# Optimization experiments

Hardware: AMD Instinct MI355X
Metric: run time of the kernel (lower is better)

## Reference

```python
import jax, jax.numpy as jnp
import numpy as np

NUM_NODE = 8192
N_PTS = 20000
FEAT_DIM = 32
POS_THRESH = 0.1
NEG_THRESH = 1.4
POS_RADIUS = 0.0375   # hardcoded literal in the original forward
NEG_RADIUS = 0.1      # hardcoded literal in the original forward
BIG = 100000.0
EPS = 1e-7


def setup_inputs() -> dict:
    key = jax.random.key(0)
    k1, k2, k3, k4, k5, k6, k7 = jax.random.split(key, 7)
    # points in a small box so pos (<0.0375) and neg (>0.1) masks are both populated
    src_pcd = jax.random.uniform(k1, (N_PTS, 3), dtype=jnp.float32) * 0.2
    tgt_pcd = jax.random.uniform(k2, (N_PTS, 3), dtype=jnp.float32) * 0.2
    src_feats = jax.random.normal(k3, (N_PTS, FEAT_DIM), dtype=jnp.float32)
    tgt_feats = jax.random.normal(k4, (N_PTS, FEAT_DIM), dtype=jnp.float32)
    correspondence = jax.random.randint(k5, (NUM_NODE, 2), 0, N_PTS, dtype=jnp.int64)
    # near-identity rigid transform so transformed src stays in the same scale regime
    rot = jnp.eye(3, dtype=jnp.float32) + 0.01 * jax.random.normal(k6, (3, 3), dtype=jnp.float32)
    trans = 0.01 * jax.random.normal(k7, (3, 1), dtype=jnp.float32)
    return {
        "src_pcd": src_pcd, "tgt_pcd": tgt_pcd,
        "src_feats": src_feats, "tgt_feats": tgt_feats,
        "correspondence": correspondence, "rot": rot, "trans": trans,
    }


def _pdist_l2(A, B):
    # GEMM form of sqrt(sum((a-b)^2) + 1e-7); same math as the broadcasted original
    d2 = (jnp.sum(A * A, axis=1)[:, None]
          + jnp.sum(B * B, axis=1)[None, :]
          - 2.0 * A @ B.T)
    return jnp.sqrt(jnp.maximum(d2, 0.0) + EPS)


def reference(src_pcd, tgt_pcd, src_feats, tgt_feats, correspondence, rot, trans):
    # rigid transform of src cloud: (R @ P^T + t)^T
    src_pcd = (rot @ src_pcd.T + trans).T
    ci = correspondence[:, 0]
    cj = correspondence[:, 1]
    sel_src_pts = src_pcd[ci]       # [N,3]
    sel_tgt_pts = tgt_pcd[cj]       # [N,3]
    sel_src_feats = src_feats[ci]   # [N,D]
    sel_tgt_feats = tgt_feats[cj]   # [N,D]

    pts_dist = _pdist_l2(sel_src_pts, sel_tgt_pts)      # [N,N]
    feats_dist = _pdist_l2(sel_src_feats, sel_tgt_feats)  # [N,N]

    pos_mask = pts_dist < POS_RADIUS
    neg_mask = pts_dist > NEG_RADIUS

    furthest_positive = jnp.max(feats_dist * pos_mask.astype(feats_dist.dtype), axis=-1)
    closest_negative = jnp.min(jnp.where(neg_mask, feats_dist, BIG), axis=-1)

    pos_loss = jax.nn.relu(furthest_positive - POS_THRESH)
    neg_loss = jax.nn.relu(NEG_THRESH - closest_negative)
    loss = pos_loss.mean() + neg_loss.mean()
    return loss
```

## Files before the change

kernel.cpp:

```cpp
#include <hip/hip_runtime.h>
#include <math.h>
#include <float.h>

#define NN 8192

typedef __bf16 bf16x8 __attribute__((ext_vector_type(8)));
typedef __bf16 bf16x4 __attribute__((ext_vector_type(4)));
typedef float f32x4 __attribute__((ext_vector_type(4)));

constexpr float POS_R2 = 0.0375f * 0.0375f;
constexpr float NEG_R2 = 0.1f * 0.1f;
constexpr float EPSF = 1e-7f;
constexpr float PRC = POS_R2 - EPSF;
constexpr float NRC = NEG_R2 - EPSF;
constexpr float POS_TH = 0.1f;
constexpr float NEG_TH = 1.4f;

#define FT_OFF 0
#define FS2_OFF (NN * 64)
#define PSX_OFF (2 * NN * 64)
#define PTX_OFF (3 * NN * 64)
#define FNS_OFF (4 * NN * 64)
#define FNT_OFF (4 * NN * 64 + NN * 4)
#define MAXB_OFF (4 * NN * 64 + 2 * NN * 4)
#define MINB_OFF (4 * NN * 64 + 3 * NN * 4)

__global__ __launch_bounds__(256) void hcl_prep(
    const float* __restrict__ src_pcd, const float* __restrict__ tgt_pcd,
    const float* __restrict__ src_feats, const float* __restrict__ tgt_feats,
    const int* __restrict__ corr, const float* __restrict__ rot,
    const float* __restrict__ trans, char* __restrict__ ws) {
  int i = blockIdx.x * 256 + threadIdx.x;
  if (i >= NN) return;
  int ci = corr[2 * i];
  int cj = corr[2 * i + 1];

  float r00 = rot[0], r01 = rot[1], r02 = rot[2];
  float r10 = rot[3], r11 = rot[4], r12 = rot[5];
  float r20 = rot[6], r21 = rot[7], r22 = rot[8];
  float t0 = trans[0], t1 = trans[1], t2 = trans[2];

  float px = src_pcd[ci * 3 + 0], py = src_pcd[ci * 3 + 1], pz = src_pcd[ci * 3 + 2];
  float qx = r00 * px + r01 * py + r02 * pz + t0;
  float qy = r10 * px + r11 * py + r12 * pz + t1;
  float qz = r20 * px + r21 * py + r22 * pz + t2;
  float sa = qx * qx + qy * qy + qz * qz;

  float ux = tgt_pcd[cj * 3 + 0], uy = tgt_pcd[cj * 3 + 1], uz = tgt_pcd[cj * 3 + 2];
  float sb = ux * ux + uy * uy + uz * uz;

  __bf16 qhx = (__bf16)qx, qhy = (__bf16)qy, qhz = (__bf16)qz;
  __bf16 qlx = (__bf16)(qx - (float)qhx);
  __bf16 qly = (__bf16)(qy - (float)qhy);
  __bf16 qlz = (__bf16)(qz - (float)qhz);
  __bf16 sah = (__bf16)sa;
  __bf16 sal = (__bf16)(sa - (float)sah);

  __bf16 uhx = (__bf16)ux, uhy = (__bf16)uy, uhz = (__bf16)uz;
  __bf16 ulx = (__bf16)(ux - (float)uhx);
  __bf16 uly = (__bf16)(uy - (float)uhy);
  __bf16 ulz = (__bf16)(uz - (float)uhz);
  __bf16 sbh = (__bf16)sb;
  __bf16 sbl = (__bf16)(sb - (float)sbh);
  __bf16 m2hx = (__bf16)(-2.f * (float)uhx), m2hy = (__bf16)(-2.f * (float)uhy),
         m2hz = (__bf16)(-2.f * (float)uhz);
  __bf16 m2lx = (__bf16)(-2.f * (float)ulx), m2ly = (__bf16)(-2.f * (float)uly),
         m2lz = (__bf16)(-2.f * (float)ulz);
  __bf16 one = (__bf16)1.0f, zero = (__bf16)0.0f;

  {
    bf16x8 v0, v1, vz;
    v0[0] = qhx; v0[1] = qhy; v0[2] = qhz; v0[3] = qhx; v0[4] = qhy; v0[5] = qhz;
    v0[6] = qlx; v0[7] = qly;
    v1[0] = qlz; v1[1] = sah; v1[2] = sal; v1[3] = one; v1[4] = one;
    v1[5] = zero; v1[6] = zero; v1[7] = zero;
    for (int k = 0; k < 8; ++k) vz[k] = zero;
    bf16x8* p = (bf16x8*)(ws + PSX_OFF + (size_t)i * 64);
    p[0] = v0; p[1] = v1; p[2] = vz; p[3] = vz;
  }
  {
    bf16x8 w0, w1, wz;
    w0[0] = m2hx; w0[1] = m2hy; w0[2] = m2hz; w0[3] = m2lx; w0[4] = m2ly; w0[5] = m2lz;
    w0[6] = m2hx; w0[7] = m2hy;
    w1[0] = m2hz; w1[1] = one; w1[2] = one; w1[3] = sbh; w1[4] = sbl;
    w1[5] = zero; w1[6] = zero; w1[7] = zero;
    for (int k = 0; k < 8; ++k) wz[k] = zero;
    bf16x8* p = (bf16x8*)(ws + PTX_OFF + (size_t)i * 64);
    p[0] = w0; p[1] = w1; p[2] = wz; p[3] = wz;
  }

  float fa = 0.f, fb = 0.f;
  const float4* sf = (const float4*)(src_feats + (size_t)ci * 32);
  const float4* tf = (const float4*)(tgt_feats + (size_t)cj * 32);
  bf16x4* ofs = (bf16x4*)(ws + FS2_OFF + (size_t)i * 64);
  bf16x4* oft = (bf16x4*)(ws + FT_OFF + (size_t)i * 64);
#pragma unroll
  for (int k = 0; k < 8; ++k) {
    float4 a = sf[k];
    __bf16 h0 = (__bf16)a.x, h1 = (__bf16)a.y, h2 = (__bf16)a.z, h3 = (__bf16)a.w;
    float f0 = (float)h0, f1 = (float)h1, f2 = (float)h2, f3 = (float)h3;
    fa += f0 * f0 + f1 * f1 + f2 * f2 + f3 * f3;
    bf16x4 o;
    o[0] = (__bf16)(-2.f * f0); o[1] = (__bf16)(-2.f * f1);
    o[2] = (__bf16)(-2.f * f2); o[3] = (__bf16)(-2.f * f3);
    ofs[k] = o;

    float4 b = tf[k];
    __bf16 g0 = (__bf16)b.x, g1 = (__bf16)b.y, g2 = (__bf16)b.z, g3 = (__bf16)b.w;
    float e0 = (float)g0, e1 = (float)g1, e2 = (float)g2, e3 = (float)g3;
    fb += e0 * e0 + e1 * e1 + e2 * e2 + e3 * e3;
    bf16x4 o2;
    o2[0] = g0; o2[1] = g1; o2[2] = g2; o2[3] = g3;
    oft[k] = o2;
  }
  ((float*)(ws + FNS_OFF))[i] = fa;
  ((float*)(ws + FNT_OFF))[i] = fb;
  ((unsigned int*)(ws + MAXB_OFF))[i] = 0u;
  ((unsigned int*)(ws + MINB_OFF))[i] = 0x7F7FFFFFu;
}

__global__ __launch_bounds__(256, 4) void hcl_dist(char* __restrict__ ws) {
  const int lane = threadIdx.x & 63;
  const int wave = threadIdx.x >> 6;
  const int quad = lane >> 4;
  const int n = lane & 15;
  const int i0 = blockIdx.y * 128 + wave * 32;
  const int j0 = blockIdx.x * 512;

  const bf16x8 afeat0 = *(const bf16x8*)(ws + FS2_OFF + (size_t)(i0 + n) * 64 + quad * 16);
  const bf16x8 afeat1 = *(const bf16x8*)(ws + FS2_OFF + (size_t)(i0 + 16 + n) * 64 + quad * 16);
  const bf16x8 apos0 = *(const bf16x8*)(ws + PSX_OFF + (size_t)(i0 + n) * 64 + quad * 16);
  const bf16x8 apos1 = *(const bf16x8*)(ws + PSX_OFF + (size_t)(i0 + 16 + n) * 64 + quad * 16);
  const f32x4 fa0 = *(const f32x4*)(ws + FNS_OFF + (size_t)(i0 + quad * 4) * 4);
  const f32x4 fa1 = *(const f32x4*)(ws + FNS_OFF + (size_t)(i0 + 16 + quad * 4) * 4);

  float maxv[8], minv[8];
#pragma unroll
  for (int r = 0; r < 8; ++r) {
    maxv[r] = -1.0f;
    minv[r] = FLT_MAX;
  }

#pragma unroll 2
  for (int s = 0; s < 32; ++s) {
    const int col = j0 + s * 16 + n;
    const bf16x8 bfeat = *(const bf16x8*)(ws + FT_OFF + (size_t)col * 64 + quad * 16);
    const bf16x8 bpos = *(const bf16x8*)(ws + PTX_OFF + (size_t)col * 64 + quad * 16);
    const float fb = *(const float*)(ws + FNT_OFF + (size_t)col * 4);

    f32x4 c0, c1, z;
    c0[0] = fa0[0] + fb; c0[1] = fa0[1] + fb; c0[2] = fa0[2] + fb; c0[3] = fa0[3] + fb;
    c1[0] = fa1[0] + fb; c1[1] = fa1[1] + fb; c1[2] = fa1[2] + fb; c1[3] = fa1[3] + fb;
    z[0] = 0.f; z[1] = 0.f; z[2] = 0.f; z[3] = 0.f;

    f32x4 d0 = __builtin_amdgcn_mfma_f32_16x16x32_bf16(afeat0, bfeat, c0, 0, 0, 0);
    f32x4 d1 = __builtin_amdgcn_mfma_f32_16x16x32_bf16(afeat1, bfeat, c1, 0, 0, 0);
    f32x4 u0 = __builtin_amdgcn_mfma_f32_16x16x32_bf16(apos0, bpos, z, 0, 0, 0);
    f32x4 u1 = __builtin_amdgcn_mfma_f32_16x16x32_bf16(apos1, bpos, z, 0, 0, 0);

#pragma unroll
    for (int r = 0; r < 4; ++r) {
      bool p0 = u0[r] < PRC, g0 = u0[r] > NRC;
      maxv[r] = fmaxf(maxv[r], p0 ? d0[r] : -1.0f);
      minv[r] = fminf(minv[r], g0 ? d0[r] : FLT_MAX);
      bool p1 = u1[r] < PRC, g1 = u1[r] > NRC;
      maxv[4 + r] = fmaxf(maxv[4 + r], p1 ? d1[r] : -1.0f);
      minv[4 + r] = fminf(minv[4 + r], g1 ? d1[r] : FLT_MAX);
    }
  }

  unsigned int* maxb = (unsigned int*)(ws + MAXB_OFF);
  unsigned int* minb = (unsigned int*)(ws + MINB_OFF);
#pragma unroll
  for (int r = 0; r < 8; ++r) {
    float mx = maxv[r], mn = minv[r];
#pragma unroll
    for (int sh = 1; sh <= 8; sh <<= 1) {
      mx = fmaxf(mx, __shfl_xor(mx, sh, 64));
      mn = fminf(mn, __shfl_xor(mn, sh, 64));
    }
    if (n == 0) {
      int row = i0 + (r < 4 ? 0 : 16) + quad * 4 + (r & 3);
      atomicMax(maxb + row, __float_as_uint(fmaxf(mx, 0.f)));
      atomicMin(minb + row, __float_as_uint(fmaxf(mn, 0.f)));
    }
  }
}

__global__ __launch_bounds__(256) void hcl_loss(const char* __restrict__ ws,
                                               float* __restrict__ out) {
  int t = threadIdx.x;
  const float* maxb = (const float*)(ws + MAXB_OFF);
  const float* minb = (const float*)(ws + MINB_OFF);
  float sp = 0.f, sn = 0.f;
#pragma unroll 8
  for (int i = t; i < NN; i += 256) {
    float fp = sqrtf(maxb[i] + EPSF);
    float cn = sqrtf(minb[i] + EPSF);
    sp += fmaxf(fp - POS_TH, 0.f);
    sn += fmaxf(NEG_TH - cn, 0.f);
  }
  __shared__ float red[8];
#pragma unroll
  for (int s = 32; s >= 1; s >>= 1) {
    sp += __shfl_down(sp, s, 64);
    sn += __shfl_down(sn, s, 64);
  }
  int wid = t >> 6;
  if ((t & 63) == 0) {
    red[wid] = sp;
    red[4 + wid] = sn;
  }
  __syncthreads();
  if (t == 0) {
    float tsp = red[0] + red[1] + red[2] + red[3];
    float tsn = red[4] + red[5] + red[6] + red[7];
    out[0] = (tsp + tsn) * (1.0f / NN);
  }
}

extern "C" void kernel_launch(void* const* d_in, const int* in_sizes, int n_in,
                              void* d_out, int out_size, void* d_ws, size_t ws_size,
                              hipStream_t stream) {
  const float* src_pcd = (const float*)d_in[0];
  const float* tgt_pcd = (const float*)d_in[1];
  const float* src_feats = (const float*)d_in[2];
  const float* tgt_feats = (const float*)d_in[3];
  const int* corr = (const int*)d_in[4];
  const float* rot = (const float*)d_in[5];
  const float* trans = (const float*)d_in[6];
  float* out = (float*)d_out;
  char* ws = (char*)d_ws;

  hcl_prep<<<NN / 256, 256, 0, stream>>>(src_pcd, tgt_pcd, src_feats, tgt_feats, corr, rot,
                                         trans, ws);
  hcl_dist<<<dim3(16, 64), 256, 0, stream>>>(ws);
  hcl_loss<<<1, 256, 0, stream>>>(ws, out);
}
```

Baseline: 104.8 us.

## Split prep work across four threads per row, unroll dist loop, vectorize loss

The prep kernel now assigns four threads to each correspondence row. Each thread converts a quarter of the features, the norms are combined with shuffles, and the point-encoding work is spread over different lanes. The dist kernel's column loop is unrolled by four with pointer increments, so loads can be issued in groups. The loss kernel reads float4 vectors. Together these aim to cut the latency of the small prep and loss kernels and the address overhead in the main loop, at the cost of some lane divergence in prep and higher register pressure in dist.

```diff
diff --git a/kernel.cpp b/kernel.cpp
--- a/kernel.cpp
+++ b/kernel.cpp
@@ -5,7 +5,6 @@
 #define NN 8192
 
 typedef __bf16 bf16x8 __attribute__((ext_vector_type(8)));
-typedef __bf16 bf16x4 __attribute__((ext_vector_type(4)));
 typedef float f32x4 __attribute__((ext_vector_type(4)));
 
 constexpr float POS_R2 = 0.0375f * 0.0375f;
@@ -30,93 +29,99 @@
     const float* __restrict__ src_feats, const float* __restrict__ tgt_feats,
     const int* __restrict__ corr, const float* __restrict__ rot,
     const float* __restrict__ trans, char* __restrict__ ws) {
-  int i = blockIdx.x * 256 + threadIdx.x;
-  if (i >= NN) return;
+  int t = blockIdx.x * 256 + threadIdx.x;
+  int i = t >> 2;
+  int p = t & 3;
   int ci = corr[2 * i];
   int cj = corr[2 * i + 1];
 
-  float r00 = rot[0], r01 = rot[1], r02 = rot[2];
-  float r10 = rot[3], r11 = rot[4], r12 = rot[5];
-  float r20 = rot[6], r21 = rot[7], r22 = rot[8];
-  float t0 = trans[0], t1 = trans[1], t2 = trans[2];
-
-  float px = src_pcd[ci * 3 + 0], py = src_pcd[ci * 3 + 1], pz = src_pcd[ci * 3 + 2];
-  float qx = r00 * px + r01 * py + r02 * pz + t0;
-  float qy = r10 * px + r11 * py + r12 * pz + t1;
-  float qz = r20 * px + r21 * py + r22 * pz + t2;
-  float sa = qx * qx + qy * qy + qz * qz;
-
-  float ux = tgt_pcd[cj * 3 + 0], uy = tgt_pcd[cj * 3 + 1], uz = tgt_pcd[cj * 3 + 2];
-  float sb = ux * ux + uy * uy + uz * uz;
-
-  __bf16 qhx = (__bf16)qx, qhy = (__bf16)qy, qhz = (__bf16)qz;
-  __bf16 qlx = (__bf16)(qx - (float)qhx);
-  __bf16 qly = (__bf16)(qy - (float)qhy);
-  __bf16 qlz = (__bf16)(qz - (float)qhz);
-  __bf16 sah = (__bf16)sa;
-  __bf16 sal = (__bf16)(sa - (float)sah);
-
-  __bf16 uhx = (__bf16)ux, uhy = (__bf16)uy, uhz = (__bf16)uz;
-  __bf16 ulx = (__bf16)(ux - (float)uhx);
-  __bf16 uly = (__bf16)(uy - (float)uhy);
-  __bf16 ulz = (__bf16)(uz - (float)uhz);
-  __bf16 sbh = (__bf16)sb;
-  __bf16 sbl = (__bf16)(sb - (float)sbh);
-  __bf16 m2hx = (__bf16)(-2.f * (float)uhx), m2hy = (__bf16)(-2.f * (float)uhy),
-         m2hz = (__bf16)(-2.f * (float)uhz);
-  __bf16 m2lx = (__bf16)(-2.f * (float)ulx), m2ly = (__bf16)(-2.f * (float)uly),
-         m2lz = (__bf16)(-2.f * (float)ulz);
+  const float4* sf = (const float4*)(src_feats + (size_t)ci * 32);
+  const float4* tf = (const float4*)(tgt_feats + (size_t)cj * 32);
+  float na = 0.f, nb = 0.f;
+  bf16x8 osrc, otgt;
+#pragma unroll
+  for (int h = 0; h < 2; ++h) {
+    float4 a = sf[2 * p + h];
+    __bf16 h0 = (__bf16)a.x, h1 = (__bf16)a.y, h2 = (__bf16)a.z, h3 = (__bf16)a.w;
+    float f0 = (float)h0, f1 = (float)h1, f2 = (float)h2, f3 = (float)h3;
+    na += f0 * f0 + f1 * f1 + f2 * f2 + f3 * f3;
+    osrc[4 * h + 0] = (__bf16)(-2.f * f0);
+    osrc[4 * h + 1] = (__bf16)(-2.f * f1);
+    osrc[4 * h + 2] = (__bf16)(-2.f * f2);
+    osrc[4 * h + 3] = (__bf16)(-2.f * f3);
+
+    float4 b = tf[2 * p + h];
+    __bf16 g0 = (__bf16)b.x, g1 = (__bf16)b.y, g2 = (__bf16)b.z, g3 = (__bf16)b.w;
+    nb += (float)g0 * (float)g0 + (float)g1 * (float)g1 + (float)g2 * (float)g2 +
+          (float)g3 * (float)g3;
+    otgt[4 * h + 0] = g0;
+    otgt[4 * h + 1] = g1;
+    otgt[4 * h + 2] = g2;
+    otgt[4 * h + 3] = g3;
+  }
+  *(bf16x8*)(ws + FS2_OFF + (size_t)i * 64 + p * 16) = osrc;
+  *(bf16x8*)(ws + FT_OFF + (size_t)i * 64 + p * 16) = otgt;
+
+  na += __shfl_xor(na, 1, 4);
+  na += __shfl_xor(na, 2, 4);
+  nb += __shfl_xor(nb, 1, 4);
+  nb += __shfl_xor(nb, 2, 4);
+
   __bf16 one = (__bf16)1.0f, zero = (__bf16)0.0f;
 
-  {
+  if (p == 0) {
+    ((float*)(ws + FNS_OFF))[i] = na;
+    ((float*)(ws + FNT_OFF))[i] = nb;
+    ((unsigned int*)(ws + MAXB_OFF))[i] = 0u;
+    ((unsigned int*)(ws + MINB_OFF))[i] = 0x7F7FFFFFu;
+  } else if (p == 1) {
+    float r00 = rot[0], r01 = rot[1], r02 = rot[2];
+    float r10 = rot[3], r11 = rot[4], r12 = rot[5];
+    float r20 = rot[6], r21 = rot[7], r22 = rot[8];
+    float t0 = trans[0], t1 = trans[1], t2 = trans[2];
+    float px = src_pcd[ci * 3 + 0], py = src_pcd[ci * 3 + 1], pz = src_pcd[ci * 3 + 2];
+    float qx = r00 * px + r01 * py + r02 * pz + t0;
+    float qy = r10 * px + r11 * py + r12 * pz + t1;
+    float qz = r20 * px + r21 * py + r22 * pz + t2;
+    float sa = qx * qx + qy * qy + qz * qz;
+    __bf16 qhx = (__bf16)qx, qhy = (__bf16)qy, qhz = (__bf16)qz;
+    __bf16 qlx = (__bf16)(qx - (float)qhx);
+    __bf16 qly = (__bf16)(qy - (float)qhy);
+    __bf16 qlz = (__bf16)(qz - (float)qhz);
+    __bf16 sah = (__bf16)sa;
+    __bf16 sal = (__bf16)(sa - (float)sah);
     bf16x8 v0, v1, vz;
     v0[0] = qhx; v0[1] = qhy; v0[2] = qhz; v0[3] = qhx; v0[4] = qhy; v0[5] = qhz;
     v0[6] = qlx; v0[7] = qly;
     v1[0] = qlz; v1[1] = sah; v1[2] = sal; v1[3] = one; v1[4] = one;
     v1[5] = zero; v1[6] = zero; v1[7] = zero;
+#pragma unroll
     for (int k = 0; k < 8; ++k) vz[k] = zero;
-    bf16x8* p = (bf16x8*)(ws + PSX_OFF + (size_t)i * 64);
-    p[0] = v0; p[1] = v1; p[2] = vz; p[3] = vz;
-  }
-  {
+    bf16x8* o = (bf16x8*)(ws + PSX_OFF + (size_t)i * 64);
+    o[0] = v0; o[1] = v1; o[2] = vz; o[3] = vz;
+  } else if (p == 2) {
+    float ux = tgt_pcd[cj * 3 + 0], uy = tgt_pcd[cj * 3 + 1], uz = tgt_pcd[cj * 3 + 2];
+    float sb = ux * ux + uy * uy + uz * uz;
+    __bf16 uhx = (__bf16)ux, uhy = (__bf16)uy, uhz = (__bf16)uz;
+    __bf16 ulx = (__bf16)(ux - (float)uhx);
+    __bf16 uly = (__bf16)(uy - (float)uhy);
+    __bf16 ulz = (__bf16)(uz - (float)uhz);
+    __bf16 sbh = (__bf16)sb;
+    __bf16 sbl = (__bf16)(sb - (float)sbh);
+    __bf16 m2hx = (__bf16)(-2.f * (float)uhx), m2hy = (__bf16)(-2.f * (float)uhy),
+           m2hz = (__bf16)(-2.f * (float)uhz);
+    __bf16 m2lx = (__bf16)(-2.f * (float)ulx), m2ly = (__bf16)(-2.f * (float)uly),
+           m2lz = (__bf16)(-2.f * (float)ulz);
     bf16x8 w0, w1, wz;
     w0[0] = m2hx; w0[1] = m2hy; w0[2] = m2hz; w0[3] = m2lx; w0[4] = m2ly; w0[5] = m2lz;
     w0[6] = m2hx; w0[7] = m2hy;
     w1[0] = m2hz; w1[1] = one; w1[2] = one; w1[3] = sbh; w1[4] = sbl;
     w1[5] = zero; w1[6] = zero; w1[7] = zero;
+#pragma unroll
     for (int k = 0; k < 8; ++k) wz[k] = zero;
-    bf16x8* p = (bf16x8*)(ws + PTX_OFF + (size_t)i * 64);
-    p[0] = w0; p[1] = w1; p[2] = wz; p[3] = wz;
-  }
-
-  float fa = 0.f, fb = 0.f;
-  const float4* sf = (const float4*)(src_feats + (size_t)ci * 32);
-  const float4* tf = (const float4*)(tgt_feats + (size_t)cj * 32);
-  bf16x4* ofs = (bf16x4*)(ws + FS2_OFF + (size_t)i * 64);
-  bf16x4* oft = (bf16x4*)(ws + FT_OFF + (size_t)i * 64);
-#pragma unroll
-  for (int k = 0; k < 8; ++k) {
-    float4 a = sf[k];
-    __bf16 h0 = (__bf16)a.x, h1 = (__bf16)a.y, h2 = (__bf16)a.z, h3 = (__bf16)a.w;
-    float f0 = (float)h0, f1 = (float)h1, f2 = (float)h2, f3 = (float)h3;
-    fa += f0 * f0 + f1 * f1 + f2 * f2 + f3 * f3;
-    bf16x4 o;
-    o[0] = (__bf16)(-2.f * f0); o[1] = (__bf16)(-2.f * f1);
-    o[2] = (__bf16)(-2.f * f2); o[3] = (__bf16)(-2.f * f3);
-    ofs[k] = o;
-
-    float4 b = tf[k];
-    __bf16 g0 = (__bf16)b.x, g1 = (__bf16)b.y, g2 = (__bf16)b.z, g3 = (__bf16)b.w;
-    float e0 = (float)g0, e1 = (float)g1, e2 = (float)g2, e3 = (float)g3;
-    fb += e0 * e0 + e1 * e1 + e2 * e2 + e3 * e3;
-    bf16x4 o2;
-    o2[0] = g0; o2[1] = g1; o2[2] = g2; o2[3] = g3;
-    oft[k] = o2;
-  }
-  ((float*)(ws + FNS_OFF))[i] = fa;
-  ((float*)(ws + FNT_OFF))[i] = fb;
-  ((unsigned int*)(ws + MAXB_OFF))[i] = 0u;
-  ((unsigned int*)(ws + MINB_OFF))[i] = 0x7F7FFFFFu;
+    bf16x8* o = (bf16x8*)(ws + PTX_OFF + (size_t)i * 64);
+    o[0] = w0; o[1] = w1; o[2] = wz; o[3] = wz;
+  }
 }
 
 __global__ __launch_bounds__(256, 4) void hcl_dist(char* __restrict__ ws) {
@@ -126,11 +131,12 @@
   const int n = lane & 15;
   const int i0 = blockIdx.y * 128 + wave * 32;
   const int j0 = blockIdx.x * 512;
-
-  const bf16x8 afeat0 = *(const bf16x8*)(ws + FS2_OFF + (size_t)(i0 + n) * 64 + quad * 16);
-  const bf16x8 afeat1 = *(const bf16x8*)(ws + FS2_OFF + (size_t)(i0 + 16 + n) * 64 + quad * 16);
-  const bf16x8 apos0 = *(const bf16x8*)(ws + PSX_OFF + (size_t)(i0 + n) * 64 + quad * 16);
-  const bf16x8 apos1 = *(const bf16x8*)(ws + PSX_OFF + (size_t)(i0 + 16 + n) * 64 + quad * 16);
+  const size_t aoff = (size_t)quad * 16;
+
+  const bf16x8 afeat0 = *(const bf16x8*)(ws + FS2_OFF + (size_t)(i0 + n) * 64 + aoff);
+  const bf16x8 afeat1 = *(const bf16x8*)(ws + FS2_OFF + (size_t)(i0 + 16 + n) * 64 + aoff);
+  const bf16x8 apos0 = *(const bf16x8*)(ws + PSX_OFF + (size_t)(i0 + n) * 64 + aoff);
+  const bf16x8 apos1 = *(const bf16x8*)(ws + PSX_OFF + (size_t)(i0 + 16 + n) * 64 + aoff);
   const f32x4 fa0 = *(const f32x4*)(ws + FNS_OFF + (size_t)(i0 + quad * 4) * 4);
   const f32x4 fa1 = *(const f32x4*)(ws + FNS_OFF + (size_t)(i0 + 16 + quad * 4) * 4);
 
@@ -141,32 +147,40 @@
     minv[r] = FLT_MAX;
   }
 
-#pragma unroll 2
-  for (int s = 0; s < 32; ++s) {
-    const int col = j0 + s * 16 + n;
-    const bf16x8 bfeat = *(const bf16x8*)(ws + FT_OFF + (size_t)col * 64 + quad * 16);
-    const bf16x8 bpos = *(const bf16x8*)(ws + PTX_OFF + (size_t)col * 64 + quad * 16);
-    const float fb = *(const float*)(ws + FNT_OFF + (size_t)col * 4);
-
-    f32x4 c0, c1, z;
-    c0[0] = fa0[0] + fb; c0[1] = fa0[1] + fb; c0[2] = fa0[2] + fb; c0[3] = fa0[3] + fb;
-    c1[0] = fa1[0] + fb; c1[1] = fa1[1] + fb; c1[2] = fa1[2] + fb; c1[3] = fa1[3] + fb;
-    z[0] = 0.f; z[1] = 0.f; z[2] = 0.f; z[3] = 0.f;
-
-    f32x4 d0 = __builtin_amdgcn_mfma_f32_16x16x32_bf16(afeat0, bfeat, c0, 0, 0, 0);
-    f32x4 d1 = __builtin_amdgcn_mfma_f32_16x16x32_bf16(afeat1, bfeat, c1, 0, 0, 0);
-    f32x4 u0 = __builtin_amdgcn_mfma_f32_16x16x32_bf16(apos0, bpos, z, 0, 0, 0);
-    f32x4 u1 = __builtin_amdgcn_mfma_f32_16x16x32_bf16(apos1, bpos, z, 0, 0, 0);
-
-#pragma unroll
-    for (int r = 0; r < 4; ++r) {
-      bool p0 = u0[r] < PRC, g0 = u0[r] > NRC;
-      maxv[r] = fmaxf(maxv[r], p0 ? d0[r] : -1.0f);
-      minv[r] = fminf(minv[r], g0 ? d0[r] : FLT_MAX);
-      bool p1 = u1[r] < PRC, g1 = u1[r] > NRC;
-      maxv[4 + r] = fmaxf(maxv[4 + r], p1 ? d1[r] : -1.0f);
-      minv[4 + r] = fminf(minv[4 + r], g1 ? d1[r] : FLT_MAX);
+  const char* pF = ws + FT_OFF + (size_t)(j0 + n) * 64 + aoff;
+  const char* pP = ws + PTX_OFF + (size_t)(j0 + n) * 64 + aoff;
+  const char* pN = ws + FNT_OFF + (size_t)(j0 + n) * 4;
+
+  for (int s = 0; s < 8; ++s) {
+#pragma unroll
+    for (int u = 0; u < 4; ++u) {
+      const bf16x8 bfeat = *(const bf16x8*)(pF + u * 1024);
+      const bf16x8 bpos = *(const bf16x8*)(pP + u * 1024);
+      const float fb = *(const float*)(pN + u * 64);
+
+      f32x4 c0, c1, z;
+      c0[0] = fa0[0] + fb; c0[1] = fa0[1] + fb; c0[2] = fa0[2] + fb; c0[3] = fa0[3] + fb;
+      c1[0] = fa1[0] + fb; c1[1] = fa1[1] + fb; c1[2] = fa1[2] + fb; c1[3] = fa1[3] + fb;
+      z[0] = 0.f; z[1] = 0.f; z[2] = 0.f; z[3] = 0.f;
+
+      f32x4 d0 = __builtin_amdgcn_mfma_f32_16x16x32_bf16(afeat0, bfeat, c0, 0, 0, 0);
+      f32x4 d1 = __builtin_amdgcn_mfma_f32_16x16x32_bf16(afeat1, bfeat, c1, 0, 0, 0);
+      f32x4 u0 = __builtin_amdgcn_mfma_f32_16x16x32_bf16(apos0, bpos, z, 0, 0, 0);
+      f32x4 u1 = __builtin_amdgcn_mfma_f32_16x16x32_bf16(apos1, bpos, z, 0, 0, 0);
+
+#pragma unroll
+      for (int r = 0; r < 4; ++r) {
+        bool p0 = u0[r] < PRC, g0 = u0[r] > NRC;
+        maxv[r] = fmaxf(maxv[r], p0 ? d0[r] : -1.0f);
+        minv[r] = fminf(minv[r], g0 ? d0[r] : FLT_MAX);
+        bool p1 = u1[r] < PRC, g1 = u1[r] > NRC;
+        maxv[4 + r] = fmaxf(maxv[4 + r], p1 ? d1[r] : -1.0f);
+        minv[4 + r] = fminf(minv[4 + r], g1 ? d1[r] : FLT_MAX);
+      }
     }
+    pF += 4096;
+    pP += 4096;
+    pN += 256;
   }
 
   unsigned int* maxb = (unsigned int*)(ws + MAXB_OFF);
@@ -190,15 +204,17 @@
 __global__ __launch_bounds__(256) void hcl_loss(const char* __restrict__ ws,
                                                float* __restrict__ out) {
   int t = threadIdx.x;
-  const float* maxb = (const float*)(ws + MAXB_OFF);
-  const float* minb = (const float*)(ws + MINB_OFF);
+  const float4* maxb = (const float4*)(ws + MAXB_OFF);
+  const float4* minb = (const float4*)(ws + MINB_OFF);
   float sp = 0.f, sn = 0.f;
-#pragma unroll 8
-  for (int i = t; i < NN; i += 256) {
-    float fp = sqrtf(maxb[i] + EPSF);
-    float cn = sqrtf(minb[i] + EPSF);
-    sp += fmaxf(fp - POS_TH, 0.f);
-    sn += fmaxf(NEG_TH - cn, 0.f);
+#pragma unroll
+  for (int k = 0; k < 8; ++k) {
+    float4 mx = maxb[t + 256 * k];
+    float4 mn = minb[t + 256 * k];
+    sp += fmaxf(sqrtf(mx.x + EPSF) - POS_TH, 0.f) + fmaxf(sqrtf(mx.y + EPSF) - POS_TH, 0.f) +
+          fmaxf(sqrtf(mx.z + EPSF) - POS_TH, 0.f) + fmaxf(sqrtf(mx.w + EPSF) - POS_TH, 0.f);
+    sn += fmaxf(NEG_TH - sqrtf(mn.x + EPSF), 0.f) + fmaxf(NEG_TH - sqrtf(mn.y + EPSF), 0.f) +
+          fmaxf(NEG_TH - sqrtf(mn.z + EPSF), 0.f) + fmaxf(NEG_TH - sqrtf(mn.w + EPSF), 0.f);
   }
   __shared__ float red[8];
 #pragma unroll
@@ -232,8 +248,8 @@
   float* out = (float*)d_out;
   char* ws = (char*)d_ws;
 
-  hcl_prep<<<NN / 256, 256, 0, stream>>>(src_pcd, tgt_pcd, src_feats, tgt_feats, corr, rot,
-                                         trans, ws);
+  hcl_prep<<<NN * 4 / 256, 256, 0, stream>>>(src_pcd, tgt_pcd, src_feats, tgt_feats, corr,
+                                             rot, trans, ws);
   hcl_dist<<<dim3(16, 64), 256, 0, stream>>>(ws);
   hcl_loss<<<1, 256, 0, stream>>>(ws, out);
 }
```

Result: faster. 100.9 us (-3.7%).

## Stage column tiles in LDS, fuse loss into dist kernel, parallelize prep

Applied to the files above, without the earlier changes.

The distance kernel now loads its 512-column tile of target features, positions and norms into LDS once per block with global_load_lds, and the inner loop reads from LDS instead of global memory. Blocks grow to 512 threads covering 256 rows. The separate loss kernel is removed: the last block to finish, chosen by an atomic ticket counter, does the final reduction. The prep kernel uses 8 threads per row, and the position buffers shrink from 64 to 32 bytes per row. This removes one launch and redundant global column loads, at the cost of a grid-wide atomic and roughly 50KB of LDS per block, which limits occupancy.

```diff
diff --git a/kernel.cpp b/kernel.cpp
--- a/kernel.cpp
+++ b/kernel.cpp
@@ -19,118 +19,151 @@
 #define FT_OFF 0
 #define FS2_OFF (NN * 64)
 #define PSX_OFF (2 * NN * 64)
-#define PTX_OFF (3 * NN * 64)
-#define FNS_OFF (4 * NN * 64)
-#define FNT_OFF (4 * NN * 64 + NN * 4)
-#define MAXB_OFF (4 * NN * 64 + 2 * NN * 4)
-#define MINB_OFF (4 * NN * 64 + 3 * NN * 4)
+#define PTX_OFF (2 * NN * 64 + NN * 32)
+#define FNS_OFF (2 * NN * 64 + 2 * NN * 32)
+#define FNT_OFF (FNS_OFF + NN * 4)
+#define MAXB_OFF (FNT_OFF + NN * 4)
+#define MINB_OFF (MAXB_OFF + NN * 4)
+#define CNT_OFF (MINB_OFF + NN * 4)
+
+__device__ inline void load_lds16(const void* g, void* l) {
+  __builtin_amdgcn_global_load_lds(
+      (const __attribute__((address_space(1))) unsigned int*)g,
+      (__attribute__((address_space(3))) unsigned int*)l, 16, 0, 0);
+}
 
 __global__ __launch_bounds__(256) void hcl_prep(
     const float* __restrict__ src_pcd, const float* __restrict__ tgt_pcd,
     const float* __restrict__ src_feats, const float* __restrict__ tgt_feats,
     const int* __restrict__ corr, const float* __restrict__ rot,
     const float* __restrict__ trans, char* __restrict__ ws) {
-  int i = blockIdx.x * 256 + threadIdx.x;
-  if (i >= NN) return;
+  int t = blockIdx.x * 256 + threadIdx.x;
+  int i = t >> 3;
+  int p = t & 7;
   int ci = corr[2 * i];
   int cj = corr[2 * i + 1];
 
-  float r00 = rot[0], r01 = rot[1], r02 = rot[2];
-  float r10 = rot[3], r11 = rot[4], r12 = rot[5];
-  float r20 = rot[6], r21 = rot[7], r22 = rot[8];
-  float t0 = trans[0], t1 = trans[1], t2 = trans[2];
-
-  float px = src_pcd[ci * 3 + 0], py = src_pcd[ci * 3 + 1], pz = src_pcd[ci * 3 + 2];
-  float qx = r00 * px + r01 * py + r02 * pz + t0;
-  float qy = r10 * px + r11 * py + r12 * pz + t1;
-  float qz = r20 * px + r21 * py + r22 * pz + t2;
-  float sa = qx * qx + qy * qy + qz * qz;
-
-  float ux = tgt_pcd[cj * 3 + 0], uy = tgt_pcd[cj * 3 + 1], uz = tgt_pcd[cj * 3 + 2];
-  float sb = ux * ux + uy * uy + uz * uz;
-
-  __bf16 qhx = (__bf16)qx, qhy = (__bf16)qy, qhz = (__bf16)qz;
-  __bf16 qlx = (__bf16)(qx - (float)qhx);
-  __bf16 qly = (__bf16)(qy - (float)qhy);
-  __bf16 qlz = (__bf16)(qz - (float)qhz);
-  __bf16 sah = (__bf16)sa;
-  __bf16 sal = (__bf16)(sa - (float)sah);
-
-  __bf16 uhx = (__bf16)ux, uhy = (__bf16)uy, uhz = (__bf16)uz;
-  __bf16 ulx = (__bf16)(ux - (float)uhx);
-  __bf16 uly = (__bf16)(uy - (float)uhy);
-  __bf16 ulz = (__bf16)(uz - (float)uhz);
-  __bf16 sbh = (__bf16)sb;
-  __bf16 sbl = (__bf16)(sb - (float)sbh);
-  __bf16 m2hx = (__bf16)(-2.f * (float)uhx), m2hy = (__bf16)(-2.f * (float)uhy),
-         m2hz = (__bf16)(-2.f * (float)uhz);
-  __bf16 m2lx = (__bf16)(-2.f * (float)ulx), m2ly = (__bf16)(-2.f * (float)uly),
-         m2lz = (__bf16)(-2.f * (float)ulz);
+  float4 a = ((const float4*)(src_feats + (size_t)ci * 32))[p];
+  float4 b = ((const float4*)(tgt_feats + (size_t)cj * 32))[p];
+  __bf16 h0 = (__bf16)a.x, h1 = (__bf16)a.y, h2 = (__bf16)a.z, h3 = (__bf16)a.w;
+  float f0 = (float)h0, f1 = (float)h1, f2 = (float)h2, f3 = (float)h3;
+  float na = f0 * f0 + f1 * f1 + f2 * f2 + f3 * f3;
+  bf16x4 osrc;
+  osrc[0] = (__bf16)(-2.f * f0); osrc[1] = (__bf16)(-2.f * f1);
+  osrc[2] = (__bf16)(-2.f * f2); osrc[3] = (__bf16)(-2.f * f3);
+  __bf16 g0 = (__bf16)b.x, g1 = (__bf16)b.y, g2 = (__bf16)b.z, g3 = (__bf16)b.w;
+  float e0 = (float)g0, e1 = (float)g1, e2 = (float)g2, e3 = (float)g3;
+  float nb = e0 * e0 + e1 * e1 + e2 * e2 + e3 * e3;
+  bf16x4 otgt;
+  otgt[0] = g0; otgt[1] = g1; otgt[2] = g2; otgt[3] = g3;
+  *(bf16x4*)(ws + FS2_OFF + (size_t)i * 64 + p * 8) = osrc;
+  *(bf16x4*)(ws + FT_OFF + (size_t)i * 64 + p * 8) = otgt;
+
+  na += __shfl_xor(na, 1, 8);
+  na += __shfl_xor(na, 2, 8);
+  na += __shfl_xor(na, 4, 8);
+  nb += __shfl_xor(nb, 1, 8);
+  nb += __shfl_xor(nb, 2, 8);
+  nb += __shfl_xor(nb, 4, 8);
+
   __bf16 one = (__bf16)1.0f, zero = (__bf16)0.0f;
 
-  {
-    bf16x8 v0, v1, vz;
+  if (p == 0) {
+    ((float*)(ws + FNS_OFF))[i] = na;
+    ((float*)(ws + FNT_OFF))[i] = nb;
+    ((unsigned int*)(ws + MAXB_OFF))[i] = 0u;
+    ((unsigned int*)(ws + MINB_OFF))[i] = 0x7F7FFFFFu;
+  } else if (p == 3) {
+    if (i == 0) *(unsigned int*)(ws + CNT_OFF) = 0u;
+  } else if (p == 1) {
+    float r00 = rot[0], r01 = rot[1], r02 = rot[2];
+    float r10 = rot[3], r11 = rot[4], r12 = rot[5];
+    float r20 = rot[6], r21 = rot[7], r22 = rot[8];
+    float t0 = trans[0], t1 = trans[1], t2 = trans[2];
+    float px = src_pcd[ci * 3 + 0], py = src_pcd[ci * 3 + 1], pz = src_pcd[ci * 3 + 2];
+    float qx = r00 * px + r01 * py + r02 * pz + t0;
+    float qy = r10 * px + r11 * py + r12 * pz + t1;
+    float qz = r20 * px + r21 * py + r22 * pz + t2;
+    float sa = qx * qx + qy * qy + qz * qz;
+    __bf16 qhx = (__bf16)qx, qhy = (__bf16)qy, qhz = (__bf16)qz;
+    __bf16 qlx = (__bf16)(qx - (float)qhx);
+    __bf16 qly = (__bf16)(qy - (float)qhy);
+    __bf16 qlz = (__bf16)(qz - (float)qhz);
+    __bf16 sah = (__bf16)sa;
+    __bf16 sal = (__bf16)(sa - (float)sah);
+    bf16x8 v0, v1;
     v0[0] = qhx; v0[1] = qhy; v0[2] = qhz; v0[3] = qhx; v0[4] = qhy; v0[5] = qhz;
     v0[6] = qlx; v0[7] = qly;
     v1[0] = qlz; v1[1] = sah; v1[2] = sal; v1[3] = one; v1[4] = one;
     v1[5] = zero; v1[6] = zero; v1[7] = zero;
-    for (int k = 0; k < 8; ++k) vz[k] = zero;
-    bf16x8* p = (bf16x8*)(ws + PSX_OFF + (size_t)i * 64);
-    p[0] = v0; p[1] = v1; p[2] = vz; p[3] = vz;
-  }
-  {
-    bf16x8 w0, w1, wz;
+    bf16x8* o = (bf16x8*)(ws + PSX_OFF + (size_t)i * 32);
+    o[0] = v0;
+    o[1] = v1;
+  } else if (p == 2) {
+    float ux = tgt_pcd[cj * 3 + 0], uy = tgt_pcd[cj * 3 + 1], uz = tgt_pcd[cj * 3 + 2];
+    float sb = ux * ux + uy * uy + uz * uz;
+    __bf16 uhx = (__bf16)ux, uhy = (__bf16)uy, uhz = (__bf16)uz;
+    __bf16 ulx = (__bf16)(ux - (float)uhx);
+    __bf16 uly = (__bf16)(uy - (float)uhy);
+    __bf16 ulz = (__bf16)(uz - (float)uhz);
+    __bf16 sbh = (__bf16)sb;
+    __bf16 sbl = (__bf16)(sb - (float)sbh);
+    __bf16 m2hx = (__bf16)(-2.f * (float)uhx), m2hy = (__bf16)(-2.f * (float)uhy),
+           m2hz = (__bf16)(-2.f * (float)uhz);
+    __bf16 m2lx = (__bf16)(-2.f * (float)ulx), m2ly = (__bf16)(-2.f * (float)uly),
+           m2lz = (__bf16)(-2.f * (float)ulz);
+    bf16x8 w0, w1;
     w0[0] = m2hx; w0[1] = m2hy; w0[2] = m2hz; w0[3] = m2lx; w0[4] = m2ly; w0[5] = m2lz;
     w0[6] = m2hx; w0[7] = m2hy;
     w1[0] = m2hz; w1[1] = one; w1[2] = one; w1[3] = sbh; w1[4] = sbl;
     w1[5] = zero; w1[6] = zero; w1[7] = zero;
-    for (int k = 0; k < 8; ++k) wz[k] = zero;
-    bf16x8* p = (bf16x8*)(ws + PTX_OFF + (size_t)i * 64);
-    p[0] = w0; p[1] = w1; p[2] = wz; p[3] = wz;
-  }
-
-  float fa = 0.f, fb = 0.f;
-  const float4* sf = (const float4*)(src_feats + (size_t)ci * 32);
-  const float4* tf = (const float4*)(tgt_feats + (size_t)cj * 32);
-  bf16x4* ofs = (bf16x4*)(ws + FS2_OFF + (size_t)i * 64);
-  bf16x4* oft = (bf16x4*)(ws + FT_OFF + (size_t)i * 64);
-#pragma unroll
-  for (int k = 0; k < 8; ++k) {
-    float4 a = sf[k];
-    __bf16 h0 = (__bf16)a.x, h1 = (__bf16)a.y, h2 = (__bf16)a.z, h3 = (__bf16)a.w;
-    float f0 = (float)h0, f1 = (float)h1, f2 = (float)h2, f3 = (float)h3;
-    fa += f0 * f0 + f1 * f1 + f2 * f2 + f3 * f3;
-    bf16x4 o;
-    o[0] = (__bf16)(-2.f * f0); o[1] = (__bf16)(-2.f * f1);
-    o[2] = (__bf16)(-2.f * f2); o[3] = (__bf16)(-2.f * f3);
-    ofs[k] = o;
-
-    float4 b = tf[k];
-    __bf16 g0 = (__bf16)b.x, g1 = (__bf16)b.y, g2 = (__bf16)b.z, g3 = (__bf16)b.w;
-    float e0 = (float)g0, e1 = (float)g1, e2 = (float)g2, e3 = (float)g3;
-    fb += e0 * e0 + e1 * e1 + e2 * e2 + e3 * e3;
-    bf16x4 o2;
-    o2[0] = g0; o2[1] = g1; o2[2] = g2; o2[3] = g3;
-    oft[k] = o2;
-  }
-  ((float*)(ws + FNS_OFF))[i] = fa;
-  ((float*)(ws + FNT_OFF))[i] = fb;
-  ((unsigned int*)(ws + MAXB_OFF))[i] = 0u;
-  ((unsigned int*)(ws + MINB_OFF))[i] = 0x7F7FFFFFu;
-}
-
-__global__ __launch_bounds__(256, 4) void hcl_dist(char* __restrict__ ws) {
-  const int lane = threadIdx.x & 63;
-  const int wave = threadIdx.x >> 6;
-  const int quad = lane >> 4;
-  const int n = lane & 15;
-  const int i0 = blockIdx.y * 128 + wave * 32;
+    bf16x8* o = (bf16x8*)(ws + PTX_OFF + (size_t)i * 32);
+    o[0] = w0;
+    o[1] = w1;
+  }
+}
+
+__global__ __launch_bounds__(512, 4) void hcl_dist(char* __restrict__ ws,
+                                                   float* __restrict__ out) {
+  __shared__ char ldsF[32768];
+  __shared__ char ldsP[16384 + 64];
+  __shared__ char ldsN[2048];
+  __shared__ unsigned int s_ticket;
+  __shared__ float red[16];
+
+  const int tid = threadIdx.x;
+  const int lane = tid & 63, wv = tid >> 6;
+  const int quad = lane >> 4, n = lane & 15;
+  const int i0 = blockIdx.y * 256 + wv * 32;
   const int j0 = blockIdx.x * 512;
 
+  {
+    const char* gF = ws + FT_OFF + (size_t)j0 * 64;
+    const char* gP = ws + PTX_OFF + (size_t)j0 * 32;
+    const char* gN = ws + FNT_OFF + (size_t)j0 * 4;
+#pragma unroll
+    for (int r = 0; r < 4; ++r) {
+      int off = wv * 1024 + r * 8192;
+      load_lds16(gF + off + lane * 16, ldsF + off);
+    }
+#pragma unroll
+    for (int r = 0; r < 2; ++r) {
+      int off = wv * 1024 + r * 8192;
+      load_lds16(gP + off + lane * 16, ldsP + off);
+    }
+    if (wv == 0) load_lds16(gN + lane * 16, ldsN);
+    if (wv == 1) load_lds16(gN + 1024 + lane * 16, ldsN + 1024);
+  }
+  if (tid < 4) ((f32x4*)(ldsP + 16384))[tid] = f32x4{0.f, 0.f, 0.f, 0.f};
+
   const bf16x8 afeat0 = *(const bf16x8*)(ws + FS2_OFF + (size_t)(i0 + n) * 64 + quad * 16);
-  const bf16x8 afeat1 = *(const bf16x8*)(ws + FS2_OFF + (size_t)(i0 + 16 + n) * 64 + quad * 16);
-  const bf16x8 apos0 = *(const bf16x8*)(ws + PSX_OFF + (size_t)(i0 + n) * 64 + quad * 16);
-  const bf16x8 apos1 = *(const bf16x8*)(ws + PSX_OFF + (size_t)(i0 + 16 + n) * 64 + quad * 16);
+  const bf16x8 afeat1 =
+      *(const bf16x8*)(ws + FS2_OFF + (size_t)(i0 + 16 + n) * 64 + quad * 16);
+  bf16x8 apos0 = {}, apos1 = {};
+  if (quad < 2) {
+    apos0 = *(const bf16x8*)(ws + PSX_OFF + (size_t)(i0 + n) * 32 + quad * 16);
+    apos1 = *(const bf16x8*)(ws + PSX_OFF + (size_t)(i0 + 16 + n) * 32 + quad * 16);
+  }
   const f32x4 fa0 = *(const f32x4*)(ws + FNS_OFF + (size_t)(i0 + quad * 4) * 4);
   const f32x4 fa1 = *(const f32x4*)(ws + FNS_OFF + (size_t)(i0 + 16 + quad * 4) * 4);
 
@@ -141,12 +174,17 @@
     minv[r] = FLT_MAX;
   }
 
-#pragma unroll 2
+  asm volatile("s_waitcnt vmcnt(0)" ::: "memory");
+  __syncthreads();
+
+  const char* lF = ldsF + n * 64 + quad * 16;
+  const char* lP = ldsP + n * 32 + quad * 16;
+  const char* lN = ldsN + n * 4;
+#pragma unroll 8
   for (int s = 0; s < 32; ++s) {
-    const int col = j0 + s * 16 + n;
-    const bf16x8 bfeat = *(const bf16x8*)(ws + FT_OFF + (size_t)col * 64 + quad * 16);
-    const bf16x8 bpos = *(const bf16x8*)(ws + PTX_OFF + (size_t)col * 64 + quad * 16);
-    const float fb = *(const float*)(ws + FNT_OFF + (size_t)col * 4);
+    const bf16x8 bfeat = *(const bf16x8*)(lF + s * 1024);
+    const bf16x8 bpos = *(const bf16x8*)(lP + s * 512);
+    const float fb = *(const float*)(lN + s * 64);
 
     f32x4 c0, c1, z;
     c0[0] = fa0[0] + fb; c0[1] = fa0[1] + fb; c0[2] = fa0[2] + fb; c0[3] = fa0[3] + fb;
@@ -185,37 +223,45 @@
       atomicMin(minb + row, __float_as_uint(fmaxf(mn, 0.f)));
     }
   }
-}
-
-__global__ __launch_bounds__(256) void hcl_loss(const char* __restrict__ ws,
-                                               float* __restrict__ out) {
-  int t = threadIdx.x;
-  const float* maxb = (const float*)(ws + MAXB_OFF);
-  const float* minb = (const float*)(ws + MINB_OFF);
-  float sp = 0.f, sn = 0.f;
-#pragma unroll 8
-  for (int i = t; i < NN; i += 256) {
-    float fp = sqrtf(maxb[i] + EPSF);
-    float cn = sqrtf(minb[i] + EPSF);
-    sp += fmaxf(fp - POS_TH, 0.f);
-    sn += fmaxf(NEG_TH - cn, 0.f);
-  }
-  __shared__ float red[8];
-#pragma unroll
-  for (int s = 32; s >= 1; s >>= 1) {
-    sp += __shfl_down(sp, s, 64);
-    sn += __shfl_down(sn, s, 64);
-  }
-  int wid = t >> 6;
-  if ((t & 63) == 0) {
-    red[wid] = sp;
-    red[4 + wid] = sn;
+
+  __threadfence();
+  if (tid == 0) {
+    s_ticket = __hip_atomic_fetch_add((unsigned int*)(ws + CNT_OFF), 1u, __ATOMIC_ACQ_REL,
+                                      __HIP_MEMORY_SCOPE_AGENT);
   }
   __syncthreads();
-  if (t == 0) {
-    float tsp = red[0] + red[1] + red[2] + red[3];
-    float tsn = red[4] + red[5] + red[6] + red[7];
-    out[0] = (tsp + tsn) * (1.0f / NN);
+  if (s_ticket == 16 * 32 - 1) {
+    __threadfence();
+    float sp = 0.f, sn = 0.f;
+#pragma unroll
+    for (int k = 0; k < 16; ++k) {
+      int i = tid + 512 * k;
+      float mx = __uint_as_float(
+          __hip_atomic_load(maxb + i, __ATOMIC_RELAXED, __HIP_MEMORY_SCOPE_AGENT));
+      float mn = __uint_as_float(
+          __hip_atomic_load(minb + i, __ATOMIC_RELAXED, __HIP_MEMORY_SCOPE_AGENT));
+      sp += fmaxf(sqrtf(mx + EPSF) - POS_TH, 0.f);
+      sn += fmaxf(NEG_TH - sqrtf(mn + EPSF), 0.f);
+    }
+#pragma unroll
+    for (int sh = 32; sh >= 1; sh >>= 1) {
+      sp += __shfl_down(sp, sh, 64);
+      sn += __shfl_down(sn, sh, 64);
+    }
+    if ((tid & 63) == 0) {
+      red[wv] = sp;
+      red[8 + wv] = sn;
+    }
+    __syncthreads();
+    if (tid == 0) {
+      float tsp = 0.f, tsn = 0.f;
+#pragma unroll
+      for (int w = 0; w < 8; ++w) {
+        tsp += red[w];
+        tsn += red[8 + w];
+      }
+      out[0] = (tsp + tsn) * (1.0f / NN);
+    }
   }
 }
 
@@ -232,8 +278,7 @@
   float* out = (float*)d_out;
   char* ws = (char*)d_ws;
 
-  hcl_prep<<<NN / 256, 256, 0, stream>>>(src_pcd, tgt_pcd, src_feats, tgt_feats, corr, rot,
-                                         trans, ws);
-  hcl_dist<<<dim3(16, 64), 256, 0, stream>>>(ws);
-  hcl_loss<<<1, 256, 0, stream>>>(ws, out);
-}
+  hcl_prep<<<NN * 8 / 256, 256, 0, stream>>>(src_pcd, tgt_pcd, src_feats, tgt_feats, corr,
+                                             rot, trans, ws);
+  hcl_dist<<<dim3(16, 32), 512, 0, stream>>>(ws, out);
+}
```

Measured after the change: 151.4 us. 1.44x slower.
